# Optimization experiments

Hardware: AMD Instinct MI355X
Metric: run time of the kernel (lower is better)

Reference implementation:

```python
import math
import jax, jax.numpy as jnp
import numpy as np

NUM_GROUPS = 32
EPS = 1e-5


def setup_inputs() -> dict:
    key = jax.random.key(0)
    ks = jax.random.split(key, 4)
    b, c, h, w = 8, 512, 64, 64
    x = jax.random.normal(ks[0], (b, c, h, w), dtype=jnp.float32)
    norm_w = jnp.ones((c,), jnp.float32)
    norm_b = jnp.zeros((c,), jnp.float32)
    qkv_w = jax.random.normal(ks[1], (3 * c, c), dtype=jnp.float32) * (1.0 / math.sqrt(c))
    qkv_b = jnp.zeros((3 * c,), jnp.float32)
    out_w = jax.random.normal(ks[2], (c, c), dtype=jnp.float32) * (1.0 / math.sqrt(c))
    out_b = jnp.zeros((c,), jnp.float32)
    return {"x": x, "norm_w": norm_w, "norm_b": norm_b, "qkv_w": qkv_w,
            "qkv_b": qkv_b, "out_w": out_w, "out_b": out_b}


def reference(x, norm_w, norm_b, qkv_w, qkv_b, out_w, out_b):
    b, c, h, w = x.shape
    L = h * w
    # GroupNorm over (c/g, h, w) per group
    xg = x.reshape(b, NUM_GROUPS, -1)
    mu = xg.mean(axis=-1, keepdims=True)
    var = xg.var(axis=-1, keepdims=True)
    xn = ((xg - mu) * jax.lax.rsqrt(var + EPS)).reshape(b, c, L)
    xn = xn * norm_w[:, None] + norm_b[:, None]
    # 1x1 conv == channel matmul -> qkv [b, 3c, L]
    qkv = jnp.einsum('oc,bcl->bol', qkv_w, xn) + qkv_b[:, None]
    q, k, v = jnp.split(qkv, 3, axis=1)  # each [b, c, L]
    scale = 1.0 / math.sqrt(c)
    attn = jax.nn.softmax(jnp.einsum('bcl,bcs->bls', q, k) * scale, axis=-1)
    o = jnp.einsum('bls,bcs->bcl', attn, v)  # [b, c, L]
    o = jnp.einsum('oc,bcl->bol', out_w, o) + out_b[:, None]
    return o.reshape(b, c, h, w) + x
```

## Files before the change

### kernel.cpp

```cpp
#include <hip/hip_runtime.h>
#include <cstdint>

static constexpr int B_ = 8, C_ = 512, L_ = 4096, NG_ = 32;
static constexpr float RSCALE = 0.04419417382415922f;

using f32x4  = __attribute__((ext_vector_type(4))) float;
using bf16x8 = __attribute__((ext_vector_type(8))) short;

__device__ __forceinline__ uint16_t f2bf(float f) {
  union { float f; uint32_t u; } v{f};
  uint32_t r = (v.u + 0x7fffu + ((v.u >> 16) & 1u)) >> 16;
  return (uint16_t)r;
}

__global__ __launch_bounds__(256) void k_cvt_bf16(const float* __restrict__ in,
                                                  uint16_t* __restrict__ out, int n) {
  int i = (blockIdx.x * 256 + threadIdx.x) * 4;
  if (i + 3 < n) {
    float4 v = *(const float4*)(in + i);
    union { uint16_t s[4]; uint2 u; } o;
    o.s[0] = f2bf(v.x); o.s[1] = f2bf(v.y); o.s[2] = f2bf(v.z); o.s[3] = f2bf(v.w);
    *(uint2*)(out + i) = o.u;
  }
}

__global__ __launch_bounds__(256) void k_gnstats(const float* __restrict__ x,
                                                 float* __restrict__ mu, float* __restrict__ rs) {
  int bg = blockIdx.x;
  const float* p = x + (size_t)bg * (16 * L_);
  float s = 0.f, s2 = 0.f;
#pragma unroll 8
  for (int i = 0; i < 64; ++i) {
    float4 v = *(const float4*)(p + (threadIdx.x + i * 256) * 4);
    s  += v.x + v.y + v.z + v.w;
    s2 += v.x * v.x + v.y * v.y + v.z * v.z + v.w * v.w;
  }
  for (int o = 32; o; o >>= 1) { s += __shfl_down(s, o); s2 += __shfl_down(s2, o); }
  __shared__ float as_[4], as2_[4];
  int w = threadIdx.x >> 6;
  if ((threadIdx.x & 63) == 0) { as_[w] = s; as2_[w] = s2; }
  __syncthreads();
  if (threadIdx.x == 0) {
    float S = as_[0] + as_[1] + as_[2] + as_[3];
    float S2 = as2_[0] + as2_[1] + as2_[2] + as2_[3];
    float m = S / 65536.0f;
    float var = S2 / 65536.0f - m * m;
    mu[bg] = m; rs[bg] = rsqrtf(var + 1e-5f);
  }
}

__global__ __launch_bounds__(256) void k_normT(const float* __restrict__ x,
                                               const float* __restrict__ nw, const float* __restrict__ nb,
                                               const float* __restrict__ mu, const float* __restrict__ rs,
                                               uint16_t* __restrict__ xnT) {
  __shared__ __align__(16) uint16_t t[64][72];
  int l0 = blockIdx.x * 64, c0 = blockIdx.y * 64, b = blockIdx.z;
#pragma unroll
  for (int i = 0; i < 4; ++i) {
    int idx = threadIdx.x + i * 256;
    int row = idx >> 4, q = idx & 15;
    int c = c0 + row;
    float m_ = mu[b * NG_ + (c >> 4)], r_ = rs[b * NG_ + (c >> 4)];
    float sc = r_ * nw[c], sh = nb[c] - m_ * sc;
    float4 v = *(const float4*)(x + (size_t)(b * C_ + c) * L_ + l0 + q * 4);
    int lb = q * 4;
    t[lb + 0][row] = f2bf(v.x * sc + sh);
    t[lb + 1][row] = f2bf(v.y * sc + sh);
    t[lb + 2][row] = f2bf(v.z * sc + sh);
    t[lb + 3][row] = f2bf(v.w * sc + sh);
  }
  __syncthreads();
#pragma unroll
  for (int i = 0; i < 2; ++i) {
    int idx = threadIdx.x + i * 256;
    int row = idx >> 3, ch = idx & 7;
    uint4 v = *(const uint4*)(&t[row][ch * 8]);
    *(uint4*)(xnT + (size_t)(b * L_ + l0 + row) * C_ + c0 + ch * 8) = v;
  }
}

__global__ __launch_bounds__(256) void k_vT(const uint16_t* __restrict__ qkvT, uint16_t* __restrict__ vn) {
  __shared__ __align__(16) uint16_t t[64][72];
  int l0 = blockIdx.x * 64, c0 = blockIdx.y * 64, b = blockIdx.z;
#pragma unroll
  for (int i = 0; i < 2; ++i) {
    int idx = threadIdx.x + i * 256;
    int row = idx >> 3, ch = idx & 7;
    uint16_t v[8];
    *(uint4*)v = *(const uint4*)(qkvT + (size_t)(b * L_ + l0 + row) * 1536 + 1024 + c0 + ch * 8);
#pragma unroll
    for (int j = 0; j < 8; ++j) t[ch * 8 + j][row] = v[j];
  }
  __syncthreads();
#pragma unroll
  for (int i = 0; i < 2; ++i) {
    int idx = threadIdx.x + i * 256;
    int row = idx >> 3, ch = idx & 7;
    *(uint4*)(vn + (size_t)(b * C_ + c0 + row) * L_ + l0 + ch * 8) = *(const uint4*)(&t[row][ch * 8]);
  }
}

template <int MODE>
__global__ __launch_bounds__(256, 2) void k_gemm(const uint16_t* __restrict__ Ag, int lda, long long strideA,
                                                 const uint16_t* __restrict__ Bg, int ldb, long long strideB,
                                                 void* __restrict__ Cg, long long strideC,
                                                 const float* __restrict__ bias,
                                                 const float* __restrict__ resid) {
  __shared__ __align__(16) uint16_t Asm[128 * 64], Bsm[128 * 64];
  int b = blockIdx.z;
  int m0 = blockIdx.y * 128, n0 = blockIdx.x * 128;
  const uint16_t* A = Ag + (size_t)b * strideA;
  const uint16_t* Bp = Bg + (size_t)b * strideB;
  int lane = threadIdx.x & 63, w = threadIdx.x >> 6;
  int wm = w >> 1, wn = w & 1;
  int l15 = lane & 15, lhi = lane >> 4;
  f32x4 acc[4][4] = {};
  for (int kt = 0; kt < 512; kt += 64) {
#pragma unroll
    for (int i = 0; i < 4; ++i) {
      int idx = threadIdx.x + i * 256;
      int row = idx >> 3, cs = idx & 7, cg = cs ^ (row & 7);
      *(uint4*)(Asm + row * 64 + cs * 8) = *(const uint4*)(A + (size_t)(m0 + row) * lda + kt + cg * 8);
      *(uint4*)(Bsm + row * 64 + cs * 8) = *(const uint4*)(Bp + (size_t)(n0 + row) * ldb + kt + cg * 8);
    }
    __syncthreads();
#pragma unroll
    for (int kk = 0; kk < 2; ++kk) {
      bf16x8 af[4], bfr[4];
      int chunk = kk * 4 + lhi;
#pragma unroll
      for (int m = 0; m < 4; ++m) {
        int row = wm * 64 + m * 16 + l15;
        af[m] = *(const bf16x8*)(Asm + row * 64 + ((chunk ^ (row & 7)) << 3));
      }
#pragma unroll
      for (int n = 0; n < 4; ++n) {
        int row = wn * 64 + n * 16 + l15;
        bfr[n] = *(const bf16x8*)(Bsm + row * 64 + ((chunk ^ (row & 7)) << 3));
      }
#pragma unroll
      for (int m = 0; m < 4; ++m)
#pragma unroll
        for (int n = 0; n < 4; ++n)
          acc[m][n] = __builtin_amdgcn_mfma_f32_16x16x32_bf16(af[m], bfr[n], acc[m][n], 0, 0, 0);
    }
    __syncthreads();
  }
  if (MODE == 0) {
    uint16_t* Cp = (uint16_t*)Cg + (size_t)b * strideC;
#pragma unroll
    for (int n = 0; n < 4; ++n) {
      int col = n0 + wn * 64 + n * 16 + l15;
      float bs = bias[col];
      float scl = (col < 512) ? RSCALE : 1.0f;
#pragma unroll
      for (int m = 0; m < 4; ++m) {
        int rowb = m0 + wm * 64 + m * 16 + lhi * 4;
#pragma unroll
        for (int r = 0; r < 4; ++r)
          Cp[(size_t)(rowb + r) * 1536 + col] = f2bf((acc[m][n][r] + bs) * scl);
      }
    }
  } else {
    float* Cp = (float*)Cg + (size_t)b * strideC;
    const float* Xp = resid + (size_t)b * strideC;
#pragma unroll
    for (int m = 0; m < 4; ++m) {
      int rowb = m0 + wm * 64 + m * 16 + lhi * 4;
#pragma unroll
      for (int n = 0; n < 4; ++n) {
        int col = n0 + wn * 64 + n * 16 + l15;
#pragma unroll
        for (int r = 0; r < 4; ++r) {
          float v = acc[m][n][r] + bias[rowb + r] + Xp[(size_t)(rowb + r) * 4096 + col];
          Cp[(size_t)(rowb + r) * 4096 + col] = v;
        }
      }
    }
  }
}

__global__ __launch_bounds__(512, 2) void k_attn(const uint16_t* __restrict__ qkvT,
                                                 const uint16_t* __restrict__ vn,
                                                 uint16_t* __restrict__ ot) {
  __shared__ __align__(16) uint16_t qs[64 * 512];
  __shared__ __align__(16) uint16_t kvs[64 * 512];
  __shared__ __align__(16) uint16_t ps[64 * 64];
  __shared__ __align__(16) float redm[2][4][16], reds[2][4][16];
  __shared__ __align__(16) float mrun[64], lrun[64], alph[64];

  const int tid = threadIdx.x, lane = tid & 63, w = tid >> 6;
  const int l15 = lane & 15, lhi = lane >> 4;
  const int b = blockIdx.y, q0 = blockIdx.x * 64;
  const int nf = w & 3, mh = w >> 2;

  const uint16_t* qg = qkvT + (size_t)(b * L_ + q0) * 1536;
  const uint16_t* kg = qkvT + (size_t)b * L_ * 1536 + 512;
  const uint16_t* vg = vn + (size_t)b * C_ * L_;

#pragma unroll
  for (int i = 0; i < 8; ++i) {
    int idx = tid + i * 512;
    int row = idx >> 6, cs = idx & 63, cg = cs ^ (row & 7);
    *(uint4*)(qs + row * 512 + cs * 8) = *(const uint4*)(qg + (size_t)row * 1536 + cg * 8);
  }
  if (tid < 64) { mrun[tid] = -1e30f; lrun[tid] = 0.0f; }

  f32x4 acc[4][4] = {};

  for (int st = 0; st < 64; ++st) {
    __syncthreads();
    {
      uint4 tmp[8];
#pragma unroll
      for (int i = 0; i < 8; ++i) {
        int idx = tid + i * 512;
        int row = idx >> 6, cs = idx & 63, cg = cs ^ (row & 7);
        tmp[i] = *(const uint4*)(kg + (size_t)(st * 64 + row) * 1536 + cg * 8);
      }
#pragma unroll
      for (int i = 0; i < 8; ++i) {
        int idx = tid + i * 512;
        int row = idx >> 6, cs = idx & 63;
        *(uint4*)(kvs + row * 512 + cs * 8) = tmp[i];
      }
    }
    __syncthreads();

    f32x4 sfr[2] = {};
#pragma unroll
    for (int kc = 0; kc < 16; ++kc) {
      int chunk = kc * 4 + lhi;
      int qrow = nf * 16 + l15;
      bf16x8 bq = *(const bf16x8*)(qs + qrow * 512 + ((chunk ^ (qrow & 7)) << 3));
#pragma unroll
      for (int i = 0; i < 2; ++i) {
        int srow = (mh * 2 + i) * 16 + l15;
        bf16x8 ak = *(const bf16x8*)(kvs + srow * 512 + ((chunk ^ (srow & 7)) << 3));
        sfr[i] = __builtin_amdgcn_mfma_f32_16x16x32_bf16(ak, bq, sfr[i], 0, 0, 0);
      }
    }

    float pm = -1e30f;
#pragma unroll
    for (int i = 0; i < 2; ++i)
#pragma unroll
      for (int r = 0; r < 4; ++r) pm = fmaxf(pm, sfr[i][r]);
    pm = fmaxf(pm, __shfl_xor(pm, 16));
    pm = fmaxf(pm, __shfl_xor(pm, 32));
    if (lhi == 0) redm[mh][nf][l15] = pm;
    __syncthreads();

    uint4 vtmp[8];
#pragma unroll
    for (int i = 0; i < 8; ++i) {
      int idx = tid + i * 512;
      int row = idx >> 3, cs = idx & 7, cg = cs ^ (row & 7);
      vtmp[i] = *(const uint4*)(vg + (size_t)row * L_ + st * 64 + cg * 8);
    }

    float m_old = mrun[nf * 16 + l15];
    float tm = fmaxf(redm[0][nf][l15], redm[1][nf][l15]);
    float m_new = fmaxf(m_old, tm);
    float p[2][4];
    float psum = 0.f;
#pragma unroll
    for (int i = 0; i < 2; ++i)
#pragma unroll
      for (int r = 0; r < 4; ++r) { p[i][r] = __expf(sfr[i][r] - m_new); psum += p[i][r]; }
    psum += __shfl_xor(psum, 16);
    psum += __shfl_xor(psum, 32);
    if (lhi == 0) reds[mh][nf][l15] = psum;

    {
      int l = nf * 16 + l15;
#pragma unroll
      for (int i = 0; i < 2; ++i) {
        int s0 = (mh * 2 + i) * 16 + lhi * 4;
        union { uint16_t h[4]; uint2 u; } pk;
#pragma unroll
        for (int r = 0; r < 4; ++r) pk.h[r] = f2bf(p[i][r]);
        int chunk = s0 >> 3, off = s0 & 7;
        *(uint2*)(ps + l * 64 + ((chunk ^ (l & 7)) << 3) + off) = pk.u;
      }
    }
#pragma unroll
    for (int i = 0; i < 8; ++i) {
      int idx = tid + i * 512;
      int row = idx >> 3, cs = idx & 7;
      *(uint4*)(kvs + row * 64 + cs * 8) = vtmp[i];
    }
    __syncthreads();

    if (tid < 64) {
      float mo = mrun[tid];
      float tmax = fmaxf(redm[0][tid >> 4][tid & 15], redm[1][tid >> 4][tid & 15]);
      float mn = fmaxf(mo, tmax);
      float a = __expf(mo - mn);
      float tsum = reds[0][tid >> 4][tid & 15] + reds[1][tid >> 4][tid & 15];
      lrun[tid] = lrun[tid] * a + tsum;
      mrun[tid] = mn;
      alph[tid] = a;
    }
    __syncthreads();

#pragma unroll
    for (int m = 0; m < 4; ++m) {
      f32x4 a4 = *(const f32x4*)(&alph[m * 16 + lhi * 4]);
#pragma unroll
      for (int n = 0; n < 4; ++n)
#pragma unroll
        for (int r = 0; r < 4; ++r) acc[m][n][r] *= a4[r];
    }
#pragma unroll
    for (int kk = 0; kk < 2; ++kk) {
      int chunk = kk * 4 + lhi;
      bf16x8 pa[4], vb[4];
#pragma unroll
      for (int m = 0; m < 4; ++m) {
        int row = m * 16 + l15;
        pa[m] = *(const bf16x8*)(ps + row * 64 + ((chunk ^ (row & 7)) << 3));
      }
#pragma unroll
      for (int n = 0; n < 4; ++n) {
        int row = w * 64 + n * 16 + l15;
        vb[n] = *(const bf16x8*)(kvs + row * 64 + ((chunk ^ (row & 7)) << 3));
      }
#pragma unroll
      for (int m = 0; m < 4; ++m)
#pragma unroll
        for (int n = 0; n < 4; ++n)
          acc[m][n] = __builtin_amdgcn_mfma_f32_16x16x32_bf16(pa[m], vb[n], acc[m][n], 0, 0, 0);
    }
  }

#pragma unroll
  for (int m = 0; m < 4; ++m) {
    f32x4 lr = *(const f32x4*)(&lrun[m * 16 + lhi * 4]);
    f32x4 inv;
#pragma unroll
    for (int r = 0; r < 4; ++r) inv[r] = 1.0f / lr[r];
#pragma unroll
    for (int n = 0; n < 4; ++n) {
      int c = w * 64 + n * 16 + l15;
#pragma unroll
      for (int r = 0; r < 4; ++r) {
        int l = q0 + m * 16 + lhi * 4 + r;
        ot[(size_t)(b * L_ + l) * C_ + c] = f2bf(acc[m][n][r] * inv[r]);
      }
    }
  }
}

extern "C" void kernel_launch(void* const* d_in, const int* in_sizes, int n_in,
                              void* d_out, int out_size, void* d_ws, size_t ws_size,
                              hipStream_t stream) {
  const float* x  = (const float*)d_in[0];
  const float* nw = (const float*)d_in[1];
  const float* nb = (const float*)d_in[2];
  const float* qw = (const float*)d_in[3];
  const float* qb = (const float*)d_in[4];
  const float* ow = (const float*)d_in[5];
  const float* ob = (const float*)d_in[6];
  float* out = (float*)d_out;
  char* ws = (char*)d_ws;

  float*    mu   = (float*)(ws + 0);
  float*    rs   = (float*)(ws + 1024);
  uint16_t* wq   = (uint16_t*)(ws + 4096);
  uint16_t* wo   = (uint16_t*)(ws + 4096 + 1572864);
  uint16_t* xnT  = (uint16_t*)(ws + 2101248);
  uint16_t* qkvT = (uint16_t*)(ws + 35655680);
  uint16_t* vn   = (uint16_t*)(ws + 136318976);
  uint16_t* otb  = (uint16_t*)(ws + 169873408);

  k_cvt_bf16<<<dim3((1536 * 512) / 1024), 256, 0, stream>>>(qw, wq, 1536 * 512);
  k_cvt_bf16<<<dim3((512 * 512) / 1024), 256, 0, stream>>>(ow, wo, 512 * 512);
  k_gnstats<<<dim3(256), 256, 0, stream>>>(x, mu, rs);
  k_normT<<<dim3(64, 8, 8), 256, 0, stream>>>(x, nw, nb, mu, rs, xnT);
  k_gemm<0><<<dim3(12, 32, 8), 256, 0, stream>>>(xnT, 512, (long long)4096 * 512,
                                                 wq, 512, 0LL,
                                                 qkvT, (long long)4096 * 1536, qb, nullptr);
  k_vT<<<dim3(64, 8, 8), 256, 0, stream>>>(qkvT, vn);
  k_attn<<<dim3(64, 8), 512, 0, stream>>>(qkvT, vn, otb);
  k_gemm<1><<<dim3(32, 4, 8), 256, 0, stream>>>(wo, 512, 0LL,
                                                otb, 512, (long long)4096 * 512,
                                                out, (long long)512 * 4096, ob, x);
}
```

Before: 756.0 us.

## Double-buffer K tiles, keep Q and V fragments in registers in attention

The attention kernel now holds each wave's Q fragments in registers instead of shared memory and double-buffers K tiles in shared memory. The next K tile is prefetched while the current QK^T runs. V fragments are read straight from global memory into registers rather than staged through LDS. Running max and sum move into per-thread registers, removing one block barrier per iteration. The cost is more register pressure under 512-thread launch bounds and uncoalesced strided V loads from global memory.

```diff
diff --git a/kernel.cpp b/kernel.cpp
--- a/kernel.cpp
+++ b/kernel.cpp
@@ -183,11 +183,10 @@
 __global__ __launch_bounds__(512, 2) void k_attn(const uint16_t* __restrict__ qkvT,
                                                  const uint16_t* __restrict__ vn,
                                                  uint16_t* __restrict__ ot) {
-  __shared__ __align__(16) uint16_t qs[64 * 512];
-  __shared__ __align__(16) uint16_t kvs[64 * 512];
+  __shared__ __align__(16) uint16_t kbuf[2][64 * 512];
   __shared__ __align__(16) uint16_t ps[64 * 64];
   __shared__ __align__(16) float redm[2][4][16], reds[2][4][16];
-  __shared__ __align__(16) float mrun[64], lrun[64], alph[64];
+  __shared__ __align__(16) float alph[64];
 
   const int tid = threadIdx.x, lane = tid & 63, w = tid >> 6;
   const int l15 = lane & 15, lhi = lane >> 4;
@@ -196,74 +195,71 @@
 
   const uint16_t* qg = qkvT + (size_t)(b * L_ + q0) * 1536;
   const uint16_t* kg = qkvT + (size_t)b * L_ * 1536 + 512;
-  const uint16_t* vg = vn + (size_t)b * C_ * L_;
+  const uint16_t* vg = vn + (size_t)b * C_ * L_ + (size_t)(w * 64) * L_;
+
+  bf16x8 qr[16];
+  {
+    const uint16_t* qrow = qg + (size_t)(nf * 16 + l15) * 1536 + lhi * 8;
+#pragma unroll
+    for (int kc = 0; kc < 16; ++kc) qr[kc] = *(const bf16x8*)(qrow + kc * 32);
+  }
+
+  float mrun = -1e30f, lrun = 0.0f;
+  f32x4 acc[4][4] = {};
 
 #pragma unroll
   for (int i = 0; i < 8; ++i) {
-    int idx = tid + i * 512;
-    int row = idx >> 6, cs = idx & 63, cg = cs ^ (row & 7);
-    *(uint4*)(qs + row * 512 + cs * 8) = *(const uint4*)(qg + (size_t)row * 1536 + cg * 8);
-  }
-  if (tid < 64) { mrun[tid] = -1e30f; lrun[tid] = 0.0f; }
-
-  f32x4 acc[4][4] = {};
+    int row = w * 8 + i;
+    bf16x8 t = *(const bf16x8*)(kg + (size_t)row * 1536 + lane * 8);
+    *(bf16x8*)(kbuf[0] + row * 512 + ((lane ^ (row & 7)) << 3)) = t;
+  }
+  __syncthreads();
 
   for (int st = 0; st < 64; ++st) {
-    __syncthreads();
-    {
-      uint4 tmp[8];
-#pragma unroll
-      for (int i = 0; i < 8; ++i) {
-        int idx = tid + i * 512;
-        int row = idx >> 6, cs = idx & 63, cg = cs ^ (row & 7);
-        tmp[i] = *(const uint4*)(kg + (size_t)(st * 64 + row) * 1536 + cg * 8);
-      }
-#pragma unroll
-      for (int i = 0; i < 8; ++i) {
-        int idx = tid + i * 512;
-        int row = idx >> 6, cs = idx & 63;
-        *(uint4*)(kvs + row * 512 + cs * 8) = tmp[i];
-      }
-    }
-    __syncthreads();
+    const uint16_t* kcur = kbuf[st & 1];
+    uint16_t* knxt = kbuf[(st + 1) & 1];
+    const int stn = (st + 1) & 63;
+
+    bf16x8 ktmp[8];
+#pragma unroll
+    for (int i = 0; i < 8; ++i) {
+      int row = w * 8 + i;
+      ktmp[i] = *(const bf16x8*)(kg + (size_t)(stn * 64 + row) * 1536 + lane * 8);
+    }
 
     f32x4 sfr[2] = {};
 #pragma unroll
     for (int kc = 0; kc < 16; ++kc) {
       int chunk = kc * 4 + lhi;
-      int qrow = nf * 16 + l15;
-      bf16x8 bq = *(const bf16x8*)(qs + qrow * 512 + ((chunk ^ (qrow & 7)) << 3));
 #pragma unroll
       for (int i = 0; i < 2; ++i) {
         int srow = (mh * 2 + i) * 16 + l15;
-        bf16x8 ak = *(const bf16x8*)(kvs + srow * 512 + ((chunk ^ (srow & 7)) << 3));
-        sfr[i] = __builtin_amdgcn_mfma_f32_16x16x32_bf16(ak, bq, sfr[i], 0, 0, 0);
-      }
-    }
-
-    float pm = -1e30f;
-#pragma unroll
-    for (int i = 0; i < 2; ++i)
-#pragma unroll
-      for (int r = 0; r < 4; ++r) pm = fmaxf(pm, sfr[i][r]);
+        bf16x8 ak = *(const bf16x8*)(kcur + srow * 512 + ((chunk ^ (srow & 7)) << 3));
+        sfr[i] = __builtin_amdgcn_mfma_f32_16x16x32_bf16(ak, qr[kc], sfr[i], 0, 0, 0);
+      }
+    }
+
+    float pm = fmaxf(fmaxf(fmaxf(sfr[0][0], sfr[0][1]), fmaxf(sfr[0][2], sfr[0][3])),
+                     fmaxf(fmaxf(sfr[1][0], sfr[1][1]), fmaxf(sfr[1][2], sfr[1][3])));
     pm = fmaxf(pm, __shfl_xor(pm, 16));
     pm = fmaxf(pm, __shfl_xor(pm, 32));
     if (lhi == 0) redm[mh][nf][l15] = pm;
+
+#pragma unroll
+    for (int i = 0; i < 8; ++i) {
+      int row = w * 8 + i;
+      *(bf16x8*)(knxt + row * 512 + ((lane ^ (row & 7)) << 3)) = ktmp[i];
+    }
+
     __syncthreads();
 
-    uint4 vtmp[8];
-#pragma unroll
-    for (int i = 0; i < 8; ++i) {
-      int idx = tid + i * 512;
-      int row = idx >> 3, cs = idx & 7, cg = cs ^ (row & 7);
-      vtmp[i] = *(const uint4*)(vg + (size_t)row * L_ + st * 64 + cg * 8);
-    }
-
-    float m_old = mrun[nf * 16 + l15];
+    float m_old = mrun;
     float tm = fmaxf(redm[0][nf][l15], redm[1][nf][l15]);
     float m_new = fmaxf(m_old, tm);
-    float p[2][4];
-    float psum = 0.f;
+    float alpha = __expf(m_old - m_new);
+    if (w < 4 && lhi == 0) alph[nf * 16 + l15] = alpha;
+
+    float p[2][4], psum = 0.f;
 #pragma unroll
     for (int i = 0; i < 2; ++i)
 #pragma unroll
@@ -284,25 +280,19 @@
         *(uint2*)(ps + l * 64 + ((chunk ^ (l & 7)) << 3) + off) = pk.u;
       }
     }
-#pragma unroll
-    for (int i = 0; i < 8; ++i) {
-      int idx = tid + i * 512;
-      int row = idx >> 3, cs = idx & 7;
-      *(uint4*)(kvs + row * 64 + cs * 8) = vtmp[i];
-    }
+
+    bf16x8 vb[2][4];
+#pragma unroll
+    for (int kk = 0; kk < 2; ++kk)
+#pragma unroll
+      for (int n = 0; n < 4; ++n)
+        vb[kk][n] = *(const bf16x8*)(vg + (size_t)(n * 16 + l15) * L_ + st * 64 + kk * 32 + lhi * 8);
+
+    mrun = m_new;
+
     __syncthreads();
 
-    if (tid < 64) {
-      float mo = mrun[tid];
-      float tmax = fmaxf(redm[0][tid >> 4][tid & 15], redm[1][tid >> 4][tid & 15]);
-      float mn = fmaxf(mo, tmax);
-      float a = __expf(mo - mn);
-      float tsum = reds[0][tid >> 4][tid & 15] + reds[1][tid >> 4][tid & 15];
-      lrun[tid] = lrun[tid] * a + tsum;
-      mrun[tid] = mn;
-      alph[tid] = a;
-    }
-    __syncthreads();
+    lrun = lrun * alpha + (reds[0][nf][l15] + reds[1][nf][l15]);
 
 #pragma unroll
     for (int m = 0; m < 4; ++m) {
@@ -312,31 +302,30 @@
 #pragma unroll
         for (int r = 0; r < 4; ++r) acc[m][n][r] *= a4[r];
     }
+
 #pragma unroll
     for (int kk = 0; kk < 2; ++kk) {
       int chunk = kk * 4 + lhi;
-      bf16x8 pa[4], vb[4];
+      bf16x8 pa[4];
 #pragma unroll
       for (int m = 0; m < 4; ++m) {
         int row = m * 16 + l15;
         pa[m] = *(const bf16x8*)(ps + row * 64 + ((chunk ^ (row & 7)) << 3));
       }
 #pragma unroll
-      for (int n = 0; n < 4; ++n) {
-        int row = w * 64 + n * 16 + l15;
-        vb[n] = *(const bf16x8*)(kvs + row * 64 + ((chunk ^ (row & 7)) << 3));
-      }
-#pragma unroll
       for (int m = 0; m < 4; ++m)
 #pragma unroll
         for (int n = 0; n < 4; ++n)
-          acc[m][n] = __builtin_amdgcn_mfma_f32_16x16x32_bf16(pa[m], vb[n], acc[m][n], 0, 0, 0);
-    }
-  }
-
+          acc[m][n] = __builtin_amdgcn_mfma_f32_16x16x32_bf16(pa[m], vb[kk][n], acc[m][n], 0, 0, 0);
+    }
+  }
+
+  __syncthreads();
+  if (w < 4 && lhi == 0) alph[nf * 16 + l15] = lrun;
+  __syncthreads();
 #pragma unroll
   for (int m = 0; m < 4; ++m) {
-    f32x4 lr = *(const f32x4*)(&lrun[m * 16 + lhi * 4]);
+    f32x4 lr = *(const f32x4*)(&alph[m * 16 + lhi * 4]);
     f32x4 inv;
 #pragma unroll
     for (int r = 0; r < 4; ++r) inv[r] = 1.0f / lr[r];
```

Result: faster. 661.8 us (-12.5%).
